# Kernel tuning notes

Measured on AMD Instinct MI355X. Metric: run time of the kernel, lower is better.

Reference implementation:

```python
import jax, jax.numpy as jnp
import numpy as np

N = 50000        # nodes
E = 800000       # edges (pre self-loops)
H = 1            # heads
D = 64           # out_channels (incl. Lorentz time coord)
IN = 128         # in_channels
C = 1.0          # curvature c (Lorentz k)
EPS = 1e-6
NEG = 0.2        # leaky_relu negative slope


def segment_softmax(logits, seg, n):
    # numerically stable softmax over edges grouped by destination node
    m = jax.ops.segment_max(logits, seg, num_segments=n)
    m = jnp.where(jnp.isfinite(m), m, 0.0)
    e = jnp.exp(logits - m[seg])
    s = jax.ops.segment_sum(e, seg, num_segments=n)
    return e / (s[seg] + 1e-16)


def setup_inputs() -> dict:
    key = jax.random.key(0)
    k1, k2, k3, k4, k5 = jax.random.split(key, 5)
    x = jax.random.normal(k1, (N, IN), jnp.float32)
    fan = IN + H * (D - 1)
    W = jax.random.uniform(k2, (IN, H * (D - 1)), jnp.float32, -1.0, 1.0) * (6.0 / fan) ** 0.5
    b = jnp.zeros((H * (D - 1),), jnp.float32)
    att = jax.random.uniform(k3, (1, H, 2 * D), jnp.float32, -1.0, 1.0) * (6.0 / (H + 2 * D)) ** 0.5
    # random edges with no self loops (module removes them then re-adds canonical loops)
    src = jax.random.randint(k4, (E,), 0, N, jnp.int32)
    off = jax.random.randint(k5, (E,), 1, N, jnp.int32)
    dst = (src + off) % N
    edge_index = jnp.stack([src, dst], axis=0)
    return {"x": x, "W": W, "b": b, "att": att, "edge_index": edge_index}


def reference(x, W, b, att, edge_index):
    sqrt_c = C ** 0.5
    # add self loops
    loops = jnp.arange(N, dtype=edge_index.dtype)
    ei = jnp.concatenate([edge_index, jnp.stack([loops, loops])], axis=1)
    i, j = ei[0], ei[1]

    # hy_linear (plain Linear on Lorentz branch), then project to hyperboloid
    xs = (x @ W + b).reshape(N, H, D - 1)                       # space coords
    t = jnp.sqrt(jnp.sum(xs * xs, -1, keepdims=True) + C)       # time coord
    ox = jnp.concatenate([t, xs], -1)                           # (N,H,D) on manifold

    # Lorentz logmap0: d0 * (0, xs/||xs||), d0 = sqrt(c)*arccosh(x0/sqrt(c))
    nrm = jnp.sqrt(jnp.sum(xs * xs, -1, keepdims=True) + 1e-15)
    d0 = sqrt_c * jnp.arccosh(jnp.maximum(t / sqrt_c, 1.0 + EPS))
    log_x = jnp.concatenate([jnp.zeros_like(t), d0 * xs / nrm], -1)  # (N,H,D)

    x_i, x_j = log_x[i], log_x[j]        # (E2,H,D) edge gathers
    ox_i, ox_j = ox[i], ox[j]

    # attention logits
    alpha = jnp.sum(jnp.concatenate([x_i, x_j], -1) * att, -1)  # (E2,H)

    # distance-aware weighting: sqdist = c * arccosh(-<x,y>_L / c)^2
    inner = -ox_i[..., 0] * ox_j[..., 0] + jnp.sum(ox_i[..., 1:] * ox_j[..., 1:], -1)
    sqd = C * jnp.arccosh(jnp.maximum(-inner / C, 1.0 + EPS)) ** 2
    alpha = alpha * segment_softmax(sqd, i, N)

    alpha = jnp.where(alpha >= 0, alpha, NEG * alpha)           # leaky_relu
    alpha = segment_softmax(alpha, i, N)                        # (E2,H)

    out = jax.ops.segment_sum(alpha[..., None] * x_j, i, num_segments=N)  # (N,H,D)

    # proj_tan0 -> act -> proj_tan0
    out = out.at[..., 0].set(0.0)
    out = jax.nn.relu(out)
    out = out.at[..., 0].set(0.0)

    # expmap0 then projx
    usp = out[..., 1:]
    un = jnp.sqrt(jnp.sum(usp * usp, -1, keepdims=True) + 1e-15)
    sp = sqrt_c * jnp.sinh(un / sqrt_c) * usp / un
    time = jnp.sqrt(jnp.sum(sp * sp, -1, keepdims=True) + C)    # projx recomputes time
    y = jnp.concatenate([time, sp], -1)
    return y.reshape(N, H * D)
```

## Files before the change

### kernel.cpp

```cpp
#include <hip/hip_runtime.h>
#include <math.h>

#define NN 50000
#define EE 800000
#define ETOT 850000
#define INF 128
#define DD 64
#define CAP 64
#define NB_NODE ((NN + 63) / 64)
#define NB_EDGE ((ETOT + 255) / 256)
#define XP 65
#define TP 67

__device__ __forceinline__ float wsum64(float v) {
#pragma unroll
    for (int m = 1; m < 64; m <<= 1) v += __shfl_xor(v, m, 64);
    return v;
}
__device__ __forceinline__ float rlf(float v, int k) {
    return __int_as_float(__builtin_amdgcn_readlane(__float_as_int(v), k));
}

__device__ __forceinline__ float mink_full(const float* __restrict__ ox,
                                           int j, float xnv) {
    const float4* ojp = (const float4*)(ox + (size_t)(unsigned)j * DD);
    float4 oj[16];
#pragma unroll
    for (int q = 0; q < 16; ++q) oj[q] = ojp[q];
    float p0 = 0.f, p1 = 0.f, p2 = 0.f, p3 = 0.f;
#pragma unroll
    for (int q = 0; q < 16; ++q) {
        p0 = fmaf(rlf(xnv, 4 * q + 0), oj[q].x, p0);
        p1 = fmaf(rlf(xnv, 4 * q + 1), oj[q].y, p1);
        p2 = fmaf(rlf(xnv, 4 * q + 2), oj[q].z, p2);
        p3 = fmaf(rlf(xnv, 4 * q + 3), oj[q].w, p3);
    }
    return (p0 + p1 + p2 + p3) - 2.f * rlf(xnv, 0) * oj[0].x;
}

template<int NC>
__device__ __forceinline__ void gemm_q(const float* __restrict__ S,
                                       const float* __restrict__ W,
                                       int c0, int lane, float* acc) {
#pragma unroll 4
    for (int k = 0; k < INF; ++k) {
        float xk = S[k * XP + lane];
        const float* wr = W + (size_t)k * 63 + c0;
#pragma unroll
        for (int c = 0; c < NC; ++c) acc[c] = fmaf(xk, wr[c], acc[c]);
    }
}

__global__ __launch_bounds__(256) void k_node(
    const float* __restrict__ x, const float* __restrict__ W,
    const float* __restrict__ b, const float* __restrict__ att,
    float* __restrict__ ox, float* __restrict__ ai, float2* __restrict__ snd)
{
    __shared__ float S[INF * XP];
    __shared__ float PP0[256], PP1[256], PP2[256];

    const int tid  = threadIdx.x;
    const int lane = tid & 63;
    const int h    = __builtin_amdgcn_readfirstlane(tid >> 6);
    const int c0   = 16 * h;
    const int n0   = blockIdx.x * 64;
    const int n    = n0 + lane;

    for (int r = 0; r < 32; ++r) {
        int e = r * 256 + tid;
        int node = e >> 7, k = e & 127;
        int gn = min(n0 + node, NN - 1);
        S[k * XP + node] = x[(size_t)gn * INF + k];
    }
    __syncthreads();

    float acc[16];
#pragma unroll
    for (int c = 0; c < 16; ++c) acc[c] = 0.f;
    if (h < 3) gemm_q<16>(S, W, c0, lane, acc);
    else       gemm_q<15>(S, W, c0, lane, acc);
    const int nc = (h == 3) ? 15 : 16;

    float ssp = 0.f;
#pragma unroll
    for (int c = 0; c < 16; ++c) {
        if (c < nc) {
            acc[c] += b[c0 + c];
            ssp = fmaf(acc[c], acc[c], ssp);
        }
    }
    PP0[tid] = ssp;
    __syncthreads();
    float ss = PP0[lane] + PP0[64 + lane] + PP0[128 + lane] + PP0[192 + lane];

    float t   = sqrtf(ss + 1.0f);
    float nrm = sqrtf(ss + 1e-15f);
    float d0  = acoshf(fmaxf(t, 1.0f + 1e-6f));
    float scl = d0 / nrm;

    float aip = 0.f, ajp = 0.f;
#pragma unroll
    for (int c = 0; c < 16; ++c) {
        if (c < nc) {
            float lxv = scl * acc[c];
            aip = fmaf(lxv, att[1 + c0 + c], aip);
            ajp = fmaf(lxv, att[DD + 1 + c0 + c], ajp);
        }
    }
    PP1[tid] = aip; PP2[tid] = ajp;

#pragma unroll
    for (int c = 0; c < 16; ++c)
        if (c < nc) S[lane * TP + 1 + c0 + c] = acc[c];
    if (h == 0) S[lane * TP + 0] = t;
    __syncthreads();

    if (h == 0 && n < NN) {
        float aiv = PP1[lane] + PP1[64 + lane] + PP1[128 + lane] + PP1[192 + lane];
        float ajv = PP2[lane] + PP2[64 + lane] + PP2[128 + lane] + PP2[192 + lane];
        ai[n] = aiv;
        snd[n] = make_float2(ajv, scl);
    }

    for (int r = 0; r < 16; ++r) {
        int e = r * 256 + tid;
        int node = e >> 6, d = e & 63;
        if (n0 + node < NN)
            ox[(size_t)(n0 + node) * DD + d] = S[node * TP + d];
    }
}

__global__ __launch_bounds__(256) void k_place(
    const int* __restrict__ ei0, const int* __restrict__ ei1,
    int* __restrict__ cnt, int* __restrict__ colPad)
{
    int e = blockIdx.x * 256 + threadIdx.x;
    if (e >= ETOT) return;
    int i, j;
    if (e < EE) { i = ei0[e]; j = ei1[e]; }
    else        { i = e - EE; j = i; }
    int pos = atomicAdd(&cnt[i], 1);
    if (pos < CAP) colPad[(size_t)i * CAP + pos] = j;
}

__global__ __launch_bounds__(256) void k_fused(
    const int* __restrict__ cnt, const int* __restrict__ colPad,
    const float* __restrict__ ox, const float* __restrict__ ai,
    const float2* __restrict__ snd, float* __restrict__ y)
{
    const int lane = threadIdx.x & 63;
    const int wid  = threadIdx.x >> 6;
    const int n = blockIdx.x * 4 + wid;
    if (n >= NN) return;

    const int base = n * CAP;
    int deg = cnt[n];
    if (deg > CAP) deg = CAP;
    const float aii = ai[n];
    const float xnv = ox[(size_t)n * DD + lane];

    const bool act = lane < deg;
    const int  ecl = min(lane, deg - 1);
    const int  jreg = colPad[base + ecl];
    const float2 sv = snd[jreg];

    float inner = mink_full(ox, jreg, xnv);
    float arg = fmaxf(-inner, 1.0f + 1e-6f);
    float dd0 = acoshf(arg);
    float sq  = dd0 * dd0;

    float e1 = act ? expf(sq) : 0.f;
    float s1 = wsum64(e1) + 1e-16f;
    float al = (aii + sv.x) * e1 / s1;
    al = (al >= 0.f) ? al : 0.2f * al;
    float p2 = act ? expf(al) : 0.f;
    float s2 = wsum64(p2);
    float w2 = p2 / (s2 + 1e-16f) * sv.y;

    float acc = 0.f;
    int k = 0;
    for (; k + 8 <= deg; k += 8) {
        float w0 = __shfl(w2, k + 0, 64), w1 = __shfl(w2, k + 1, 64);
        float w2b = __shfl(w2, k + 2, 64), w3 = __shfl(w2, k + 3, 64);
        float w4 = __shfl(w2, k + 4, 64), w5 = __shfl(w2, k + 5, 64);
        float w6 = __shfl(w2, k + 6, 64), w7 = __shfl(w2, k + 7, 64);
        int j0 = __shfl(jreg, k + 0, 64), j1 = __shfl(jreg, k + 1, 64);
        int j2 = __shfl(jreg, k + 2, 64), j3 = __shfl(jreg, k + 3, 64);
        int j4 = __shfl(jreg, k + 4, 64), j5 = __shfl(jreg, k + 5, 64);
        int j6 = __shfl(jreg, k + 6, 64), j7 = __shfl(jreg, k + 7, 64);
        float v0 = ox[(size_t)j0 * DD + lane], v1 = ox[(size_t)j1 * DD + lane];
        float v2 = ox[(size_t)j2 * DD + lane], v3 = ox[(size_t)j3 * DD + lane];
        float v4 = ox[(size_t)j4 * DD + lane], v5 = ox[(size_t)j5 * DD + lane];
        float v6 = ox[(size_t)j6 * DD + lane], v7 = ox[(size_t)j7 * DD + lane];
        acc = fmaf(w0, v0, acc);  acc = fmaf(w1, v1, acc);
        acc = fmaf(w2b, v2, acc); acc = fmaf(w3, v3, acc);
        acc = fmaf(w4, v4, acc);  acc = fmaf(w5, v5, acc);
        acc = fmaf(w6, v6, acc);  acc = fmaf(w7, v7, acc);
    }
    for (; k < deg; ++k) {
        float w = __shfl(w2, k, 64);
        int   j = __shfl(jreg, k, 64);
        acc = fmaf(w, ox[(size_t)j * DD + lane], acc);
    }

    float usp = (lane == 0) ? 0.f : fmaxf(acc, 0.f);
    float ss = wsum64(usp * usp);
    float un = sqrtf(ss + 1e-15f);
    float sc = sinhf(un) / un;
    float sp = sc * usp;
    float time = sqrtf(sc * sc * ss + 1.0f);
    y[(size_t)n * DD + lane] = (lane == 0) ? time : sp;
}

extern "C" void kernel_launch(void* const* d_in, const int* in_sizes, int n_in,
                              void* d_out, int out_size, void* d_ws, size_t ws_size,
                              hipStream_t stream) {
    const float* x   = (const float*)d_in[0];
    const float* W   = (const float*)d_in[1];
    const float* b   = (const float*)d_in[2];
    const float* att = (const float*)d_in[3];
    const int*   ei  = (const int*)d_in[4];
    const int* ei0 = ei;
    const int* ei1 = ei + EE;
    float* out = (float*)d_out;

    float*  ws  = (float*)d_ws;
    float*  ox  = ws;
    float*  ai  = ox + (size_t)NN * DD;
    float2* snd = (float2*)(ai + NN);
    int*    cnt    = (int*)(snd + NN);
    int*    colPad = cnt + NN;

    hipMemsetAsync(cnt, 0, sizeof(int) * NN, stream);

    k_place<<<NB_EDGE, 256, 0, stream>>>(ei0, ei1, cnt, colPad);
    k_node<<<NB_NODE, 256, 0, stream>>>(x, W, b, att, ox, ai, snd);
    k_fused<<<(NN + 3) / 4, 256, 0, stream>>>(cnt, colPad, ox, ai, snd, out);
}
```

Measured before the change: 150.5 us.

## Add low-degree fast path gathering each neighbor row once as float4 slices

For nodes with degree at most 32, which is the common case given about 17 edges per node, the fused kernel splits the wavefront into 4 groups of 16 lanes. Each group loads neighbor rows as float4 slices, computes the Minkowski inner product with a 16-lane shuffle reduction, and reuses the same registers for the weighted aggregation. This replaces the old path, which loaded each neighbor row twice: once per-lane in full for the distance and again per-column for the sum. The new path costs more registers and shuffles, and the original code is kept as a fallback for higher degrees.

Result: slower. 186.2 us (+23.8%).

```diff
diff --git a/kernel.cpp b/kernel.cpp
--- a/kernel.cpp
+++ b/kernel.cpp
@@ -157,59 +157,171 @@
     int deg = cnt[n];
     if (deg > CAP) deg = CAP;
     const float aii = ai[n];
-    const float xnv = ox[(size_t)n * DD + lane];
-
-    const bool act = lane < deg;
-    const int  ecl = min(lane, deg - 1);
-    const int  jreg = colPad[base + ecl];
-    const float2 sv = snd[jreg];
-
-    float inner = mink_full(ox, jreg, xnv);
-    float arg = fmaxf(-inner, 1.0f + 1e-6f);
-    float dd0 = acoshf(arg);
-    float sq  = dd0 * dd0;
-
-    float e1 = act ? expf(sq) : 0.f;
-    float s1 = wsum64(e1) + 1e-16f;
-    float al = (aii + sv.x) * e1 / s1;
-    al = (al >= 0.f) ? al : 0.2f * al;
-    float p2 = act ? expf(al) : 0.f;
-    float s2 = wsum64(p2);
-    float w2 = p2 / (s2 + 1e-16f) * sv.y;
-
-    float acc = 0.f;
-    int k = 0;
-    for (; k + 8 <= deg; k += 8) {
-        float w0 = __shfl(w2, k + 0, 64), w1 = __shfl(w2, k + 1, 64);
-        float w2b = __shfl(w2, k + 2, 64), w3 = __shfl(w2, k + 3, 64);
-        float w4 = __shfl(w2, k + 4, 64), w5 = __shfl(w2, k + 5, 64);
-        float w6 = __shfl(w2, k + 6, 64), w7 = __shfl(w2, k + 7, 64);
-        int j0 = __shfl(jreg, k + 0, 64), j1 = __shfl(jreg, k + 1, 64);
-        int j2 = __shfl(jreg, k + 2, 64), j3 = __shfl(jreg, k + 3, 64);
-        int j4 = __shfl(jreg, k + 4, 64), j5 = __shfl(jreg, k + 5, 64);
-        int j6 = __shfl(jreg, k + 6, 64), j7 = __shfl(jreg, k + 7, 64);
-        float v0 = ox[(size_t)j0 * DD + lane], v1 = ox[(size_t)j1 * DD + lane];
-        float v2 = ox[(size_t)j2 * DD + lane], v3 = ox[(size_t)j3 * DD + lane];
-        float v4 = ox[(size_t)j4 * DD + lane], v5 = ox[(size_t)j5 * DD + lane];
-        float v6 = ox[(size_t)j6 * DD + lane], v7 = ox[(size_t)j7 * DD + lane];
-        acc = fmaf(w0, v0, acc);  acc = fmaf(w1, v1, acc);
-        acc = fmaf(w2b, v2, acc); acc = fmaf(w3, v3, acc);
-        acc = fmaf(w4, v4, acc);  acc = fmaf(w5, v5, acc);
-        acc = fmaf(w6, v6, acc);  acc = fmaf(w7, v7, acc);
-    }
-    for (; k < deg; ++k) {
-        float w = __shfl(w2, k, 64);
-        int   j = __shfl(jreg, k, 64);
-        acc = fmaf(w, ox[(size_t)j * DD + lane], acc);
-    }
-
-    float usp = (lane == 0) ? 0.f : fmaxf(acc, 0.f);
-    float ss = wsum64(usp * usp);
-    float un = sqrtf(ss + 1e-15f);
-    float sc = sinhf(un) / un;
-    float sp = sc * usp;
-    float time = sqrtf(sc * sc * ss + 1.0f);
-    y[(size_t)n * DD + lane] = (lane == 0) ? time : sp;
+
+    if (deg <= 32) {
+        const int s = lane & 15;
+        const int g = lane >> 4;
+
+        float4 xf = *(const float4*)(ox + (size_t)n * DD + 4 * s);
+        if (s == 0) xf.x = -xf.x;
+
+        const int  ecl = min(lane, deg - 1);
+        const int  jreg = colPad[base + ecl];
+        const float2 sv = snd[jreg];
+
+        const int nst = (deg + 3) >> 2;
+        int js[8]; float ajs[8], scs[8], pt[8], e1[8], w[8];
+        float4 fr[8];
+
+#pragma unroll
+        for (int t = 0; t < 8; ++t) {
+            if (t < nst) {
+                int e = 4 * t + g;
+                int ec = min(e, deg - 1);
+                js[t]  = __shfl(jreg, ec, 64);
+                ajs[t] = __shfl(sv.x, ec, 64);
+                scs[t] = __shfl(sv.y, ec, 64);
+            }
+        }
+#pragma unroll
+        for (int t = 0; t < 8; ++t) {
+            if (t < nst)
+                fr[t] = *(const float4*)(ox + (size_t)(unsigned)js[t] * DD + 4 * s);
+        }
+#pragma unroll
+        for (int t = 0; t < 8; ++t) {
+            if (t < nst) {
+                float p = xf.x * fr[t].x;
+                p = fmaf(xf.y, fr[t].y, p);
+                p = fmaf(xf.z, fr[t].z, p);
+                p = fmaf(xf.w, fr[t].w, p);
+                p += __shfl_xor(p, 1, 64);
+                p += __shfl_xor(p, 2, 64);
+                p += __shfl_xor(p, 4, 64);
+                p += __shfl_xor(p, 8, 64);
+                pt[t] = p;
+            }
+        }
+        float s1p = 0.f;
+#pragma unroll
+        for (int t = 0; t < 8; ++t) {
+            if (t < nst) {
+                int e = 4 * t + g;
+                float arg = fmaxf(-pt[t], 1.0f + 1e-6f);
+                float dd0 = acoshf(arg);
+                float v = (e < deg) ? expf(dd0 * dd0) : 0.f;
+                e1[t] = v;
+                s1p += v;
+            }
+        }
+        s1p += __shfl_xor(s1p, 16, 64);
+        s1p += __shfl_xor(s1p, 32, 64);
+        const float inv1 = 1.f / (s1p + 1e-16f);
+        float s2p = 0.f;
+#pragma unroll
+        for (int t = 0; t < 8; ++t) {
+            if (t < nst) {
+                int e = 4 * t + g;
+                float al = (aii + ajs[t]) * e1[t] * inv1;
+                al = (al >= 0.f) ? al : 0.2f * al;
+                float v = (e < deg) ? expf(al) : 0.f;
+                w[t] = v;
+                s2p += v;
+            }
+        }
+        s2p += __shfl_xor(s2p, 16, 64);
+        s2p += __shfl_xor(s2p, 32, 64);
+        const float inv2 = 1.f / (s2p + 1e-16f);
+        float4 a4 = make_float4(0.f, 0.f, 0.f, 0.f);
+#pragma unroll
+        for (int t = 0; t < 8; ++t) {
+            if (t < nst) {
+                float wt = w[t] * inv2 * scs[t];
+                a4.x = fmaf(wt, fr[t].x, a4.x);
+                a4.y = fmaf(wt, fr[t].y, a4.y);
+                a4.z = fmaf(wt, fr[t].z, a4.z);
+                a4.w = fmaf(wt, fr[t].w, a4.w);
+            }
+        }
+        a4.x += __shfl_xor(a4.x, 16, 64); a4.x += __shfl_xor(a4.x, 32, 64);
+        a4.y += __shfl_xor(a4.y, 16, 64); a4.y += __shfl_xor(a4.y, 32, 64);
+        a4.z += __shfl_xor(a4.z, 16, 64); a4.z += __shfl_xor(a4.z, 32, 64);
+        a4.w += __shfl_xor(a4.w, 16, 64); a4.w += __shfl_xor(a4.w, 32, 64);
+
+        float u0 = (s == 0) ? 0.f : fmaxf(a4.x, 0.f);
+        float u1 = fmaxf(a4.y, 0.f);
+        float u2 = fmaxf(a4.z, 0.f);
+        float u3 = fmaxf(a4.w, 0.f);
+        float ssl = u0 * u0 + u1 * u1 + u2 * u2 + u3 * u3;
+        ssl += __shfl_xor(ssl, 1, 64);
+        ssl += __shfl_xor(ssl, 2, 64);
+        ssl += __shfl_xor(ssl, 4, 64);
+        ssl += __shfl_xor(ssl, 8, 64);
+        float un = sqrtf(ssl + 1e-15f);
+        float sc = sinhf(un) / un;
+        float time = sqrtf(sc * sc * ssl + 1.0f);
+        if (g == 0) {
+            float4 o;
+            o.x = (s == 0) ? time : sc * u0;
+            o.y = sc * u1;
+            o.z = sc * u2;
+            o.w = sc * u3;
+            *(float4*)(y + (size_t)n * DD + 4 * s) = o;
+        }
+    } else {
+        const float xnv = ox[(size_t)n * DD + lane];
+        const bool act = lane < deg;
+        const int  ecl = min(lane, deg - 1);
+        const int  jreg = colPad[base + ecl];
+        const float2 sv = snd[jreg];
+
+        float inner = mink_full(ox, jreg, xnv);
+        float arg = fmaxf(-inner, 1.0f + 1e-6f);
+        float dd0 = acoshf(arg);
+        float sq  = dd0 * dd0;
+
+        float e1 = act ? expf(sq) : 0.f;
+        float s1 = wsum64(e1) + 1e-16f;
+        float al = (aii + sv.x) * e1 / s1;
+        al = (al >= 0.f) ? al : 0.2f * al;
+        float p2 = act ? expf(al) : 0.f;
+        float s2 = wsum64(p2);
+        float w2 = p2 / (s2 + 1e-16f) * sv.y;
+
+        float acc = 0.f;
+        int k = 0;
+        for (; k + 8 <= deg; k += 8) {
+            float w0 = __shfl(w2, k + 0, 64), w1 = __shfl(w2, k + 1, 64);
+            float w2b = __shfl(w2, k + 2, 64), w3 = __shfl(w2, k + 3, 64);
+            float w4 = __shfl(w2, k + 4, 64), w5 = __shfl(w2, k + 5, 64);
+            float w6 = __shfl(w2, k + 6, 64), w7 = __shfl(w2, k + 7, 64);
+            int j0 = __shfl(jreg, k + 0, 64), j1 = __shfl(jreg, k + 1, 64);
+            int j2 = __shfl(jreg, k + 2, 64), j3 = __shfl(jreg, k + 3, 64);
+            int j4 = __shfl(jreg, k + 4, 64), j5 = __shfl(jreg, k + 5, 64);
+            int j6 = __shfl(jreg, k + 6, 64), j7 = __shfl(jreg, k + 7, 64);
+            float v0 = ox[(size_t)j0 * DD + lane], v1 = ox[(size_t)j1 * DD + lane];
+            float v2 = ox[(size_t)j2 * DD + lane], v3 = ox[(size_t)j3 * DD + lane];
+            float v4 = ox[(size_t)j4 * DD + lane], v5 = ox[(size_t)j5 * DD + lane];
+            float v6 = ox[(size_t)j6 * DD + lane], v7 = ox[(size_t)j7 * DD + lane];
+            acc = fmaf(w0, v0, acc);  acc = fmaf(w1, v1, acc);
+            acc = fmaf(w2b, v2, acc); acc = fmaf(w3, v3, acc);
+            acc = fmaf(w4, v4, acc);  acc = fmaf(w5, v5, acc);
+            acc = fmaf(w6, v6, acc);  acc = fmaf(w7, v7, acc);
+        }
+        for (; k < deg; ++k) {
+            float w = __shfl(w2, k, 64);
+            int   j = __shfl(jreg, k, 64);
+            acc = fmaf(w, ox[(size_t)j * DD + lane], acc);
+        }
+
+        float usp = (lane == 0) ? 0.f : fmaxf(acc, 0.f);
+        float ss = wsum64(usp * usp);
+        float un = sqrtf(ss + 1e-15f);
+        float sc = sinhf(un) / un;
+        float sp = sc * usp;
+        float time = sqrtf(sc * sc * ss + 1.0f);
+        y[(size_t)n * DD + lane] = (lane == 0) ? time : sp;
+    }
 }
 
 extern "C" void kernel_launch(void* const* d_in, const int* in_sizes, int n_in,
```

## Fuse edge placement into node GEMM kernel and chunk K to shrink LDS

Applied to the files above, without the earlier changes.

Merges the edge-bucketing kernel into the node-transform kernel as extra blocks in one grid, so the two independent phases can run concurrently and one launch is removed. The node GEMM now stages x in two K-chunks of 64, which cuts shared memory from 128x65 to 64x67 floats and should allow more resident blocks. The cost is an extra pair of barriers and a second staging pass per block, and the heterogeneous blocks in one grid may balance unevenly.

Result: faster. 133.5 us (-11.3%).

```diff
diff --git a/kernel.cpp b/kernel.cpp
--- a/kernel.cpp
+++ b/kernel.cpp
@@ -9,6 +9,7 @@
 #define CAP 64
 #define NB_NODE ((NN + 63) / 64)
 #define NB_EDGE ((ETOT + 255) / 256)
+#define KCH 64
 #define XP 65
 #define TP 67
 
@@ -41,23 +42,37 @@
 template<int NC>
 __device__ __forceinline__ void gemm_q(const float* __restrict__ S,
                                        const float* __restrict__ W,
-                                       int c0, int lane, float* acc) {
+                                       int k0, int c0, int lane, float* acc) {
 #pragma unroll 4
-    for (int k = 0; k < INF; ++k) {
+    for (int k = 0; k < KCH; ++k) {
         float xk = S[k * XP + lane];
-        const float* wr = W + (size_t)k * 63 + c0;
+        const float* wr = W + (size_t)(k0 + k) * 63 + c0;
 #pragma unroll
         for (int c = 0; c < NC; ++c) acc[c] = fmaf(xk, wr[c], acc[c]);
     }
 }
 
-__global__ __launch_bounds__(256) void k_node(
+__global__ __launch_bounds__(256) void k_node_place(
     const float* __restrict__ x, const float* __restrict__ W,
     const float* __restrict__ b, const float* __restrict__ att,
-    float* __restrict__ ox, float* __restrict__ ai, float2* __restrict__ snd)
+    const int* __restrict__ ei0, const int* __restrict__ ei1,
+    float* __restrict__ ox, float* __restrict__ ai, float2* __restrict__ snd,
+    int* __restrict__ cnt, int* __restrict__ colPad)
 {
-    __shared__ float S[INF * XP];
+    __shared__ float S[DD * TP];
     __shared__ float PP0[256], PP1[256], PP2[256];
+
+    if (blockIdx.x >= NB_NODE) {
+        int e = (blockIdx.x - NB_NODE) * 256 + threadIdx.x;
+        if (e < ETOT) {
+            int i, j;
+            if (e < EE) { i = ei0[e]; j = ei1[e]; }
+            else        { i = e - EE; j = i; }
+            int pos = atomicAdd(&cnt[i], 1);
+            if (pos < CAP) colPad[(size_t)i * CAP + pos] = j;
+        }
+        return;
+    }
 
     const int tid  = threadIdx.x;
     const int lane = tid & 63;
@@ -66,19 +81,22 @@
     const int n0   = blockIdx.x * 64;
     const int n    = n0 + lane;
 
-    for (int r = 0; r < 32; ++r) {
-        int e = r * 256 + tid;
-        int node = e >> 7, k = e & 127;
-        int gn = min(n0 + node, NN - 1);
-        S[k * XP + node] = x[(size_t)gn * INF + k];
-    }
-    __syncthreads();
-
     float acc[16];
 #pragma unroll
     for (int c = 0; c < 16; ++c) acc[c] = 0.f;
-    if (h < 3) gemm_q<16>(S, W, c0, lane, acc);
-    else       gemm_q<15>(S, W, c0, lane, acc);
+
+    for (int k0 = 0; k0 < INF; k0 += KCH) {
+        __syncthreads();
+        for (int r = 0; r < 16; ++r) {
+            int e = r * 256 + tid;
+            int node = e >> 6, k = e & 63;
+            int gn = min(n0 + node, NN - 1);
+            S[k * XP + node] = x[(size_t)gn * INF + k0 + k];
+        }
+        __syncthreads();
+        if (h < 3) gemm_q<16>(S, W, k0, c0, lane, acc);
+        else       gemm_q<15>(S, W, k0, c0, lane, acc);
+    }
     const int nc = (h == 3) ? 15 : 16;
 
     float ssp = 0.f;
@@ -128,19 +146,6 @@
         if (n0 + node < NN)
             ox[(size_t)(n0 + node) * DD + d] = S[node * TP + d];
     }
-}
-
-__global__ __launch_bounds__(256) void k_place(
-    const int* __restrict__ ei0, const int* __restrict__ ei1,
-    int* __restrict__ cnt, int* __restrict__ colPad)
-{
-    int e = blockIdx.x * 256 + threadIdx.x;
-    if (e >= ETOT) return;
-    int i, j;
-    if (e < EE) { i = ei0[e]; j = ei1[e]; }
-    else        { i = e - EE; j = i; }
-    int pos = atomicAdd(&cnt[i], 1);
-    if (pos < CAP) colPad[(size_t)i * CAP + pos] = j;
 }
 
 __global__ __launch_bounds__(256) void k_fused(
@@ -233,7 +238,8 @@
 
     hipMemsetAsync(cnt, 0, sizeof(int) * NN, stream);
 
-    k_place<<<NB_EDGE, 256, 0, stream>>>(ei0, ei1, cnt, colPad);
-    k_node<<<NB_NODE, 256, 0, stream>>>(x, W, b, att, ox, ai, snd);
+    k_node_place<<<NB_NODE + NB_EDGE, 256, 0, stream>>>(
+        x, W, b, att, ei0, ei1, ox, ai, snd, cnt, colPad);
+
     k_fused<<<(NN + 3) / 4, 256, 0, stream>>>(cnt, colPad, ox, ai, snd, out);
 }
```
